# Optimization experiments

Measured on AMD Instinct MI355X. Metric: run time of the kernel, lower is better.

The kernel has to match this reference:

```python
import jax, jax.numpy as jnp
import numpy as np

N_NODES = 50000
N_EDGES = 800000
D_IN, D_HID, D_OUT = 128, 256, 128


def _glorot(key, shape):
    fan_in, fan_out = shape[1], shape[0]
    lim = (6.0 / (fan_in + fan_out)) ** 0.5
    return jax.random.uniform(key, shape, jnp.float32, -lim, lim)


def setup_inputs() -> dict:
    key = jax.random.key(0)
    ks = jax.random.split(key, 8)
    x = jax.random.normal(ks[0], (N_NODES, D_IN), dtype=jnp.float32)
    edge_index = jax.random.randint(ks[1], (2, N_EDGES), 0, N_NODES, dtype=jnp.int64)
    # Layer 1: SAGEConv(D_IN -> D_HID); Layer 2: SAGEConv(D_HID -> D_OUT)
    # PyG SAGEConv: out = lin_l(mean_aggr(x_j)) + lin_r(x); bias lives in lin_l.
    Wl1 = _glorot(ks[2], (D_HID, D_IN))
    bl1 = jnp.zeros((D_HID,), jnp.float32)
    Wr1 = _glorot(ks[3], (D_HID, D_IN))
    Wl2 = _glorot(ks[4], (D_OUT, D_HID))
    bl2 = jnp.zeros((D_OUT,), jnp.float32)
    Wr2 = _glorot(ks[5], (D_OUT, D_HID))
    return {"x": x, "Wl1": Wl1, "bl1": bl1, "Wr1": Wr1,
            "Wl2": Wl2, "bl2": bl2, "Wr2": Wr2, "edge_index": edge_index}


def _sage_conv(x, src, dst, deg_inv, Wl, bl, Wr):
    # gather source features per edge, sum into dst buckets, normalize by in-degree
    msg_sum = jax.ops.segment_sum(x[src], dst, num_segments=N_NODES)  # [N, d_in]
    mean = msg_sum * deg_inv  # mean aggregation; isolated nodes -> zeros
    return mean @ Wl.T + bl + x @ Wr.T


def reference(x, Wl1, bl1, Wr1, Wl2, bl2, Wr2, edge_index):
    src, dst = edge_index[0], edge_index[1]
    deg = jax.ops.segment_sum(jnp.ones((N_EDGES,), jnp.float32), dst,
                              num_segments=N_NODES)
    deg_inv = (1.0 / jnp.maximum(deg, 1.0))[:, None]  # [N, 1]
    h = _sage_conv(x, src, dst, deg_inv, Wl1, bl1, Wr1)
    h = jax.nn.relu(h)  # dropout is identity in eval mode
    out = _sage_conv(h, src, dst, deg_inv, Wl2, bl2, Wr2)
    return out
```

## Files before the change

kernel.cpp:

```cpp
#include <hip/hip_runtime.h>
#include <hip/hip_fp16.h>

#define N_NODES 50000
#define N_EDGES 800000
#define D_IN 128
#define D_HID 256
#define D_OUT 128
#define NCHUNK 196
#define GEMM_GRID 512

typedef _Float16 f16x8 __attribute__((ext_vector_type(8)));
typedef float f32x4 __attribute__((ext_vector_type(4)));


__device__ __forceinline__ void cvt8(const float* __restrict__ src,
                                     __half* __restrict__ dstp, int i) {
    const float4* s4 = (const float4*)src;
    float4 a = s4[i * 2];
    float4 b = s4[i * 2 + 1];
    float4 o;
    __half2* op = (__half2*)&o;
    op[0] = __float22half2_rn(make_float2(a.x, a.y));
    op[1] = __float22half2_rn(make_float2(a.z, a.w));
    op[2] = __float22half2_rn(make_float2(b.x, b.y));
    op[3] = __float22half2_rn(make_float2(b.z, b.w));
    ((float4*)dstp)[i] = o;
}

__global__ __launch_bounds__(256)
void prep_kernel(const float* __restrict__ x, __half* __restrict__ xb,
                 const float* __restrict__ Wl1, const float* __restrict__ Wr1,
                 const float* __restrict__ Wl2, const float* __restrict__ Wr2,
                 __half* __restrict__ wl1h, __half* __restrict__ wr1h,
                 __half* __restrict__ wl2h, __half* __restrict__ wr2h,
                 int* __restrict__ deg) {
    int b = blockIdx.x;
    if (b < 3125) {
        int i = b * 256 + threadIdx.x;
        cvt8(x, xb, i);
    } else if (b < 3141) {
        int i = (b - 3125) * 256 + threadIdx.x;
        cvt8(Wl1, wl1h, i);
        cvt8(Wr1, wr1h, i);
        cvt8(Wl2, wl2h, i);
        cvt8(Wr2, wr2h, i);
    } else {
        int i = (b - 3141) * 256 + threadIdx.x;
        if (i < N_NODES) deg[i] = 0;
    }
}


__global__ void deg_rank_kernel(const int* __restrict__ dst, int* __restrict__ deg,
                                int* __restrict__ rank) {
    int i = blockIdx.x * blockDim.x + threadIdx.x;
    if (i < N_EDGES) rank[i] = atomicAdd(&deg[dst[i]], 1);
}

__global__ void chunk_sum(const int* __restrict__ deg, int* __restrict__ partial) {
    __shared__ int s[256];
    int i = blockIdx.x * 256 + threadIdx.x;
    s[threadIdx.x] = (i < N_NODES) ? deg[i] : 0;
    __syncthreads();
    for (int off = 128; off > 0; off >>= 1) {
        if (threadIdx.x < off) s[threadIdx.x] += s[threadIdx.x + off];
        __syncthreads();
    }
    if (threadIdx.x == 0) partial[blockIdx.x] = s[0];
}

__global__ void scatter_scan(const int* __restrict__ deg, const int* __restrict__ partial,
                             int* __restrict__ row_ptr, float* __restrict__ deg_inv) {
    __shared__ int s[256];
    __shared__ int base_s;
    const int tid = threadIdx.x;
    const int bid = blockIdx.x;
    s[tid] = (tid < bid) ? partial[tid] : 0;
    __syncthreads();
    for (int off = 128; off > 0; off >>= 1) {
        if (tid < off) s[tid] += s[tid + off];
        __syncthreads();
    }
    if (tid == 0) base_s = s[0];
    __syncthreads();
    int i = bid * 256 + tid;
    int v = (i < N_NODES) ? deg[i] : 0;
    s[tid] = v;
    __syncthreads();
    for (int off = 1; off < 256; off <<= 1) {
        int t = (tid >= off) ? s[tid - off] : 0;
        __syncthreads();
        s[tid] += t;
        __syncthreads();
    }
    if (i < N_NODES) {
        int rp = base_s + s[tid] - v;
        row_ptr[i] = rp;
        deg_inv[i] = 1.0f / fmaxf((float)v, 1.0f);
        if (i == N_NODES - 1) row_ptr[N_NODES] = N_EDGES;
    }
}

__global__ void fill_csr(const int* __restrict__ src, const int* __restrict__ dst,
                         const int* __restrict__ rank, const int* __restrict__ row_ptr,
                         int* __restrict__ csr_src) {
    int e = blockIdx.x * blockDim.x + threadIdx.x;
    if (e < N_EDGES) {
        csr_src[row_ptr[dst[e]] + rank[e]] = src[e];
    }
}


__device__ __forceinline__ void add_row(const float4& v, float2 (&acc)[4]) {
    const __half2* hp = (const __half2*)&v;
    #pragma unroll
    for (int j = 0; j < 4; ++j) {
        float2 f = __half22float2(hp[j]);
        acc[j].x += f.x;
        acc[j].y += f.y;
    }
}

template<bool ACCUM_F32>
__device__ __forceinline__ void gather_core(const __half2* __restrict__ feat,
                                            const int* __restrict__ row_ptr,
                                            const int* __restrict__ csr_src,
                                            const float* __restrict__ deg_inv,
                                            __half2* __restrict__ outh,
                                            float* __restrict__ outf) {
    const float4* feat4 = (const float4*)feat;
    const int lane = threadIdx.x & 63;
    const int g = lane >> 4;
    const int s = lane & 15;
    const int n = blockIdx.x * 4 + (threadIdx.x >> 6);
    const int beg = row_ptr[n];
    const int end = row_ptr[n + 1];
    float2 acc[4] = {};

    int idx = (beg + lane < end) ? csr_src[beg + lane] : 0;
    int base = beg;
    while (base < end) {
        int cnt = end - base;
        if (cnt > 64) cnt = 64;
        const int nbase = base + 64;
        int nidx = (nbase + lane < end) ? csr_src[nbase + lane] : 0;

        int it = 0;
        for (; it + 16 <= cnt; it += 16) {
            int s0 = __shfl(idx, it + g);
            int s1 = __shfl(idx, it + 4 + g);
            int s2 = __shfl(idx, it + 8 + g);
            int s3 = __shfl(idx, it + 12 + g);
            float4 v0 = feat4[(size_t)s0 * 16 + s];
            float4 v1 = feat4[(size_t)s1 * 16 + s];
            float4 v2 = feat4[(size_t)s2 * 16 + s];
            float4 v3 = feat4[(size_t)s3 * 16 + s];
            add_row(v0, acc);
            add_row(v1, acc);
            add_row(v2, acc);
            add_row(v3, acc);
        }
        for (; it + 4 <= cnt; it += 4) {
            int s0 = __shfl(idx, it + g);
            float4 v0 = feat4[(size_t)s0 * 16 + s];
            add_row(v0, acc);
        }
        if (it < cnt) {
            int s0 = __shfl(idx, it + g);
            if (g < cnt - it) {
                float4 v0 = feat4[(size_t)s0 * 16 + s];
                add_row(v0, acc);
            }
        }
        idx = nidx;
        base = nbase;
    }

    #pragma unroll
    for (int j = 0; j < 4; ++j) {
        acc[j].x += __shfl_xor(acc[j].x, 16);
        acc[j].y += __shfl_xor(acc[j].y, 16);
        acc[j].x += __shfl_xor(acc[j].x, 32);
        acc[j].y += __shfl_xor(acc[j].y, 32);
    }
    if (g == 0) {
        float di = deg_inv[n];
        if (ACCUM_F32) {
            float4* orow = (float4*)(outf + (size_t)n * 128);
            float4 o0 = orow[s * 2];
            float4 o1 = orow[s * 2 + 1];
            o0.x += acc[0].x * di; o0.y += acc[0].y * di;
            o0.z += acc[1].x * di; o0.w += acc[1].y * di;
            o1.x += acc[2].x * di; o1.y += acc[2].y * di;
            o1.z += acc[3].x * di; o1.w += acc[3].y * di;
            orow[s * 2] = o0;
            orow[s * 2 + 1] = o1;
        } else {
            float4 o;
            __half2* op = (__half2*)&o;
            op[0] = __float22half2_rn(make_float2(acc[0].x * di, acc[0].y * di));
            op[1] = __float22half2_rn(make_float2(acc[1].x * di, acc[1].y * di));
            op[2] = __float22half2_rn(make_float2(acc[2].x * di, acc[2].y * di));
            op[3] = __float22half2_rn(make_float2(acc[3].x * di, acc[3].y * di));
            ((float4*)(outh + (size_t)n * 64))[s] = o;
        }
    }
}

__global__ __launch_bounds__(256)
void gather_mean_h(const __half2* __restrict__ feat, const int* __restrict__ row_ptr,
                   const int* __restrict__ csr_src, const float* __restrict__ deg_inv,
                   __half2* __restrict__ outv) {
    gather_core<false>(feat, row_ptr, csr_src, deg_inv, outv, nullptr);
}

__global__ __launch_bounds__(256)
void gather_mean_add_f32(const __half2* __restrict__ feat, const int* __restrict__ row_ptr,
                         const int* __restrict__ csr_src, const float* __restrict__ deg_inv,
                         float* __restrict__ out) {
    gather_core<true>(feat, row_ptr, csr_src, deg_inv, nullptr, out);
}


#define HPAD 264

__global__ __launch_bounds__(256, 1)
void gemm_fused(const __half* __restrict__ Aa, const __half* __restrict__ Ba,
                const __half* __restrict__ Ab, const __half* __restrict__ Bb,
                const float* __restrict__ bias1,
                const __half* __restrict__ B20, const __half* __restrict__ B21,
                const float* __restrict__ bias2,
                __half* __restrict__ P, float* __restrict__ out) {
    __shared__ __half hlds[2][16][HPAD];
    const int lane = threadIdx.x & 63;
    const int wave = threadIdx.x >> 6;
    const int quad = lane >> 4;
    const int l16 = lane & 15;
    const int koff = quad * 8;

    f16x8 bf1[2][4][4];
    #pragma unroll
    for (int p = 0; p < 2; ++p) {
        const __half* __restrict__ B = p ? Bb : Ba;
        #pragma unroll
        for (int kc = 0; kc < 4; ++kc)
            #pragma unroll
            for (int nt = 0; nt < 4; ++nt)
                bf1[p][kc][nt] = *(const f16x8*)(
                    B + (size_t)(wave * 64 + nt * 16 + l16) * D_IN + kc * 32 + koff);
    }
    float bv1[4];
    #pragma unroll
    for (int nt = 0; nt < 4; ++nt) bv1[nt] = bias1[wave * 64 + nt * 16 + l16];

    f16x8 bf20[8][2], bf21[8][2];
    #pragma unroll
    for (int kc = 0; kc < 8; ++kc)
        #pragma unroll
        for (int nt = 0; nt < 2; ++nt) {
            size_t brow = (size_t)(wave * 32 + nt * 16 + l16) * D_HID + kc * 32 + koff;
            bf20[kc][nt] = *(const f16x8*)(B20 + brow);
            bf21[kc][nt] = *(const f16x8*)(B21 + brow);
        }
    float bv2[2];
    #pragma unroll
    for (int nt = 0; nt < 2; ++nt) bv2[nt] = bias2[wave * 32 + nt * 16 + l16];

    const int NT = N_NODES / 16;
    const int g = gridDim.x;

    auto loadA = [&](int t, f16x8 (&a)[2][4]) {
        const size_t arow = (size_t)(t * 16 + l16) * D_IN + koff;
        #pragma unroll
        for (int kc = 0; kc < 4; ++kc) {
            a[0][kc] = *(const f16x8*)(Aa + arow + kc * 32);
            a[1][kc] = *(const f16x8*)(Ab + arow + kc * 32);
        }
    };

    auto step = [&](int tile, const f16x8 (&a)[2][4], int buf) {
        f32x4 acc1[4] = {};
        #pragma unroll
        for (int p = 0; p < 2; ++p)
            #pragma unroll
            for (int kc = 0; kc < 4; ++kc)
                #pragma unroll
                for (int nt = 0; nt < 4; ++nt)
                    acc1[nt] = __builtin_amdgcn_mfma_f32_16x16x32_f16(
                        a[p][kc], bf1[p][kc][nt], acc1[nt], 0, 0, 0);
        #pragma unroll
        for (int nt = 0; nt < 4; ++nt) {
            int col = wave * 64 + nt * 16 + l16;
            #pragma unroll
            for (int r = 0; r < 4; ++r)
                hlds[buf][quad * 4 + r][col] =
                    __float2half(fmaxf(acc1[nt][r] + bv1[nt], 0.f));
        }
        __syncthreads();
        f32x4 acc20[2] = {};
        f32x4 acc21[2] = {};
        #pragma unroll
        for (int kc = 0; kc < 8; ++kc) {
            f16x8 a2 = *(const f16x8*)&hlds[buf][l16][kc * 32 + koff];
            #pragma unroll
            for (int nt = 0; nt < 2; ++nt) {
                acc20[nt] = __builtin_amdgcn_mfma_f32_16x16x32_f16(
                    a2, bf20[kc][nt], acc20[nt], 0, 0, 0);
                acc21[nt] = __builtin_amdgcn_mfma_f32_16x16x32_f16(
                    a2, bf21[kc][nt], acc21[nt], 0, 0, 0);
            }
        }
        #pragma unroll
        for (int nt = 0; nt < 2; ++nt) {
            int col = wave * 32 + nt * 16 + l16;
            #pragma unroll
            for (int r = 0; r < 4; ++r) {
                int row = tile * 16 + quad * 4 + r;
                P[(size_t)row * D_OUT + col] = __float2half(acc20[nt][r]);
                out[(size_t)row * D_OUT + col] = acc21[nt][r] + bv2[nt];
            }
        }
    };

    f16x8 A0[2][4], A1[2][4];
    int tile = blockIdx.x;
    int buf = 0;
    loadA(tile, A0);
    while (true) {
        if (tile + g < NT) loadA(tile + g, A1);
        step(tile, A0, buf);
        buf ^= 1;
        tile += g;
        if (tile >= NT) break;
        if (tile + g < NT) loadA(tile + g, A0);
        step(tile, A1, buf);
        buf ^= 1;
        tile += g;
        if (tile >= NT) break;
    }
}

extern "C" void kernel_launch(void* const* d_in, const int* in_sizes, int n_in,
                              void* d_out, int out_size, void* d_ws, size_t ws_size,
                              hipStream_t stream) {
    const float* x   = (const float*)d_in[0];
    const float* Wl1 = (const float*)d_in[1];
    const float* bl1 = (const float*)d_in[2];
    const float* Wr1 = (const float*)d_in[3];
    const float* Wl2 = (const float*)d_in[4];
    const float* bl2 = (const float*)d_in[5];
    const float* Wr2 = (const float*)d_in[6];
    const int*   ei  = (const int*)d_in[7];
    const int* src = ei;
    const int* dst = ei + N_EDGES;
    float* out = (float*)d_out;

    char* w = (char*)d_ws;
    auto alloc = [&](size_t bytes) {
        char* r = w;
        w += (bytes + 255) & ~(size_t)255;
        return r;
    };
    int*     deg       = (int*)alloc((size_t)N_NODES * 4);
    int*     row_ptr   = (int*)alloc((size_t)(N_NODES + 1) * 4);
    int*     rank      = (int*)alloc((size_t)N_EDGES * 4);
    int*     partial   = (int*)alloc(NCHUNK * 4);
    int*     csr_src   = (int*)alloc((size_t)N_EDGES * 4);
    float*   deg_inv   = (float*)alloc((size_t)N_NODES * 4);
    __half2* xb        = (__half2*)alloc((size_t)N_NODES * 64 * 4);
    __half2* mean1     = (__half2*)alloc((size_t)N_NODES * 64 * 4);
    __half2* pb        = (__half2*)alloc((size_t)N_NODES * 64 * 4);
    __half*  wl1h      = (__half*)alloc(4 * 32768 * 2);
    __half*  wr1h = wl1h + 32768;
    __half*  wl2h = wr1h + 32768;
    __half*  wr2h = wl2h + 32768;

    prep_kernel<<<3337, 256, 0, stream>>>(x, (__half*)xb, Wl1, Wr1, Wl2, Wr2,
        wl1h, wr1h, wl2h, wr2h, deg);

    deg_rank_kernel<<<(N_EDGES + 255) / 256, 256, 0, stream>>>(dst, deg, rank);
    chunk_sum<<<NCHUNK, 256, 0, stream>>>(deg, partial);
    scatter_scan<<<NCHUNK, 256, 0, stream>>>(deg, partial, row_ptr, deg_inv);
    fill_csr<<<(N_EDGES + 255) / 256, 256, 0, stream>>>(src, dst, rank, row_ptr, csr_src);

    gather_mean_h<<<12500, 256, 0, stream>>>(xb, row_ptr, csr_src, deg_inv, mean1);

    gemm_fused<<<GEMM_GRID, 256, 0, stream>>>(
        (const __half*)mean1, wl1h, (const __half*)xb, wr1h, bl1,
        wl2h, wr2h, bl2, (__half*)pb, out);

    gather_mean_add_f32<<<12500, 256, 0, stream>>>(pb, row_ptr, csr_src, deg_inv, out);
}
```

Measured before the change: 239.4 us.

## Fuse layer-1 mean gather into the fused GEMM kernel via per-tile CSR gather

```diff
diff --git a/kernel.cpp b/kernel.cpp
--- a/kernel.cpp
+++ b/kernel.cpp
@@ -7,7 +7,8 @@
 #define D_HID 256
 #define D_OUT 128
 #define NCHUNK 196
-#define GEMM_GRID 512
+#define NTILES 3125
+#define FUSED_GRID 256
 
 typedef _Float16 f16x8 __attribute__((ext_vector_type(8)));
 typedef float f32x4 __attribute__((ext_vector_type(4)));
@@ -121,13 +122,11 @@
     }
 }
 
-template<bool ACCUM_F32>
-__device__ __forceinline__ void gather_core(const __half2* __restrict__ feat,
-                                            const int* __restrict__ row_ptr,
-                                            const int* __restrict__ csr_src,
-                                            const float* __restrict__ deg_inv,
-                                            __half2* __restrict__ outh,
-                                            float* __restrict__ outf) {
+
+__global__ __launch_bounds__(256)
+void gather_mean_add_f32(const __half2* __restrict__ feat, const int* __restrict__ row_ptr,
+                         const int* __restrict__ csr_src, const float* __restrict__ deg_inv,
+                         float* __restrict__ out) {
     const float4* feat4 = (const float4*)feat;
     const int lane = threadIdx.x & 63;
     const int g = lane >> 4;
@@ -185,158 +184,208 @@
     }
     if (g == 0) {
         float di = deg_inv[n];
-        if (ACCUM_F32) {
-            float4* orow = (float4*)(outf + (size_t)n * 128);
-            float4 o0 = orow[s * 2];
-            float4 o1 = orow[s * 2 + 1];
-            o0.x += acc[0].x * di; o0.y += acc[0].y * di;
-            o0.z += acc[1].x * di; o0.w += acc[1].y * di;
-            o1.x += acc[2].x * di; o1.y += acc[2].y * di;
-            o1.z += acc[3].x * di; o1.w += acc[3].y * di;
-            orow[s * 2] = o0;
-            orow[s * 2 + 1] = o1;
-        } else {
-            float4 o;
-            __half2* op = (__half2*)&o;
-            op[0] = __float22half2_rn(make_float2(acc[0].x * di, acc[0].y * di));
-            op[1] = __float22half2_rn(make_float2(acc[1].x * di, acc[1].y * di));
-            op[2] = __float22half2_rn(make_float2(acc[2].x * di, acc[2].y * di));
-            op[3] = __float22half2_rn(make_float2(acc[3].x * di, acc[3].y * di));
-            ((float4*)(outh + (size_t)n * 64))[s] = o;
-        }
-    }
-}
-
-__global__ __launch_bounds__(256)
-void gather_mean_h(const __half2* __restrict__ feat, const int* __restrict__ row_ptr,
-                   const int* __restrict__ csr_src, const float* __restrict__ deg_inv,
-                   __half2* __restrict__ outv) {
-    gather_core<false>(feat, row_ptr, csr_src, deg_inv, outv, nullptr);
-}
-
-__global__ __launch_bounds__(256)
-void gather_mean_add_f32(const __half2* __restrict__ feat, const int* __restrict__ row_ptr,
-                         const int* __restrict__ csr_src, const float* __restrict__ deg_inv,
-                         float* __restrict__ out) {
-    gather_core<true>(feat, row_ptr, csr_src, deg_inv, nullptr, out);
-}
-
-
-#define HPAD 264
-
-__global__ __launch_bounds__(256, 1)
-void gemm_fused(const __half* __restrict__ Aa, const __half* __restrict__ Ba,
-                const __half* __restrict__ Ab, const __half* __restrict__ Bb,
+        float4* orow = (float4*)(out + (size_t)n * 128);
+        float4 o0 = orow[s * 2];
+        float4 o1 = orow[s * 2 + 1];
+        o0.x += acc[0].x * di; o0.y += acc[0].y * di;
+        o0.z += acc[1].x * di; o0.w += acc[1].y * di;
+        o1.x += acc[2].x * di; o1.y += acc[2].y * di;
+        o1.z += acc[3].x * di; o1.w += acc[3].y * di;
+        orow[s * 2] = o0;
+        orow[s * 2 + 1] = o1;
+    }
+}
+
+
+__global__ __launch_bounds__(512, 2)
+void sage_fused(const __half* __restrict__ xb,
+                const __half* __restrict__ Wl1h, const __half* __restrict__ Wr1h,
                 const float* __restrict__ bias1,
                 const __half* __restrict__ B20, const __half* __restrict__ B21,
                 const float* __restrict__ bias2,
+                const int* __restrict__ row_ptr, const int* __restrict__ csr_src,
+                const float* __restrict__ deg_inv,
                 __half* __restrict__ P, float* __restrict__ out) {
-    __shared__ __half hlds[2][16][HPAD];
+    __shared__ __half ldsA[16][136];
+    __shared__ __half ldsH[16][264];
+    const float4* feat4 = (const float4*)xb;
     const int lane = threadIdx.x & 63;
     const int wave = threadIdx.x >> 6;
     const int quad = lane >> 4;
     const int l16 = lane & 15;
     const int koff = quad * 8;
 
-    f16x8 bf1[2][4][4];
+    f16x8 bf1[2][4][2];
     #pragma unroll
     for (int p = 0; p < 2; ++p) {
-        const __half* __restrict__ B = p ? Bb : Ba;
+        const __half* __restrict__ B = p ? Wr1h : Wl1h;
         #pragma unroll
         for (int kc = 0; kc < 4; ++kc)
             #pragma unroll
-            for (int nt = 0; nt < 4; ++nt)
+            for (int nt = 0; nt < 2; ++nt)
                 bf1[p][kc][nt] = *(const f16x8*)(
-                    B + (size_t)(wave * 64 + nt * 16 + l16) * D_IN + kc * 32 + koff);
-    }
-    float bv1[4];
+                    B + (size_t)(wave * 32 + nt * 16 + l16) * D_IN + kc * 32 + koff);
+    }
+    float bv1[2];
     #pragma unroll
-    for (int nt = 0; nt < 4; ++nt) bv1[nt] = bias1[wave * 64 + nt * 16 + l16];
-
-    f16x8 bf20[8][2], bf21[8][2];
+    for (int nt = 0; nt < 2; ++nt) bv1[nt] = bias1[wave * 32 + nt * 16 + l16];
+
+    f16x8 bf20[8], bf21[8];
     #pragma unroll
-    for (int kc = 0; kc < 8; ++kc)
-        #pragma unroll
-        for (int nt = 0; nt < 2; ++nt) {
-            size_t brow = (size_t)(wave * 32 + nt * 16 + l16) * D_HID + kc * 32 + koff;
-            bf20[kc][nt] = *(const f16x8*)(B20 + brow);
-            bf21[kc][nt] = *(const f16x8*)(B21 + brow);
-        }
-    float bv2[2];
-    #pragma unroll
-    for (int nt = 0; nt < 2; ++nt) bv2[nt] = bias2[wave * 32 + nt * 16 + l16];
-
-    const int NT = N_NODES / 16;
-    const int g = gridDim.x;
-
-    auto loadA = [&](int t, f16x8 (&a)[2][4]) {
-        const size_t arow = (size_t)(t * 16 + l16) * D_IN + koff;
+    for (int kc = 0; kc < 8; ++kc) {
+        size_t brow = (size_t)(wave * 16 + l16) * D_HID + kc * 32 + koff;
+        bf20[kc] = *(const f16x8*)(B20 + brow);
+        bf21[kc] = *(const f16x8*)(B21 + brow);
+    }
+    float bv2 = bias2[wave * 16 + l16];
+
+    for (int tile = blockIdx.x; tile < NTILES; tile += gridDim.x) {
+        f16x8 ax[4];
+        const size_t arow = (size_t)(tile * 16 + l16) * D_IN + koff;
+        #pragma unroll
+        for (int kc = 0; kc < 4; ++kc)
+            ax[kc] = *(const f16x8*)(xb + arow + kc * 32);
+
+        {
+            const int nb = tile * 16 + wave * 2;
+            int rp = row_ptr[nb + (lane < 2 ? lane : 2)];
+            float dv = (lane < 2) ? deg_inv[nb + lane] : 0.f;
+            const int spanBeg = __shfl(rp, 0);
+            const int spanEnd = __shfl(rp, 2);
+            int i0 = (spanBeg + lane < spanEnd) ? csr_src[spanBeg + lane] : 0;
+            int i1 = (spanBeg + 64 + lane < spanEnd) ? csr_src[spanBeg + 64 + lane] : 0;
+
+            #pragma unroll
+            for (int i = 0; i < 2; ++i) {
+                const int b = __shfl(rp, i);
+                const int e = __shfl(rp, i + 1);
+                float2 acc[4] = {};
+                if (e - spanBeg <= 128) {
+                    const int off = b - spanBeg;
+                    const int cnt = e - b;
+                    int it = 0;
+                    for (; it + 16 <= cnt; it += 16) {
+                        int p0 = off + it + quad;
+                        int p1 = p0 + 4, p2 = p0 + 8, p3 = p0 + 12;
+                        int a0 = __shfl(i0, p0 & 63), b0 = __shfl(i1, p0 & 63);
+                        int a1 = __shfl(i0, p1 & 63), b1 = __shfl(i1, p1 & 63);
+                        int a2 = __shfl(i0, p2 & 63), b2 = __shfl(i1, p2 & 63);
+                        int a3 = __shfl(i0, p3 & 63), b3 = __shfl(i1, p3 & 63);
+                        int s0 = p0 < 64 ? a0 : b0;
+                        int s1 = p1 < 64 ? a1 : b1;
+                        int s2 = p2 < 64 ? a2 : b2;
+                        int s3 = p3 < 64 ? a3 : b3;
+                        float4 v0 = feat4[(size_t)s0 * 16 + l16];
+                        float4 v1 = feat4[(size_t)s1 * 16 + l16];
+                        float4 v2 = feat4[(size_t)s2 * 16 + l16];
+                        float4 v3 = feat4[(size_t)s3 * 16 + l16];
+                        add_row(v0, acc);
+                        add_row(v1, acc);
+                        add_row(v2, acc);
+                        add_row(v3, acc);
+                    }
+                    for (; it + 4 <= cnt; it += 4) {
+                        int p0 = off + it + quad;
+                        int a0 = __shfl(i0, p0 & 63), b0 = __shfl(i1, p0 & 63);
+                        int s0 = p0 < 64 ? a0 : b0;
+                        float4 v0 = feat4[(size_t)s0 * 16 + l16];
+                        add_row(v0, acc);
+                    }
+                    if (it < cnt) {
+                        int p0 = off + it + quad;
+                        int a0 = __shfl(i0, p0 & 63), b0 = __shfl(i1, p0 & 63);
+                        int s0 = p0 < 64 ? a0 : b0;
+                        if (quad < cnt - it) {
+                            float4 v0 = feat4[(size_t)s0 * 16 + l16];
+                            add_row(v0, acc);
+                        }
+                    }
+                } else {
+                    int it = b;
+                    for (; it + 16 <= e; it += 16) {
+                        int s0 = csr_src[it + quad];
+                        int s1 = csr_src[it + 4 + quad];
+                        int s2 = csr_src[it + 8 + quad];
+                        int s3 = csr_src[it + 12 + quad];
+                        float4 v0 = feat4[(size_t)s0 * 16 + l16];
+                        float4 v1 = feat4[(size_t)s1 * 16 + l16];
+                        float4 v2 = feat4[(size_t)s2 * 16 + l16];
+                        float4 v3 = feat4[(size_t)s3 * 16 + l16];
+                        add_row(v0, acc);
+                        add_row(v1, acc);
+                        add_row(v2, acc);
+                        add_row(v3, acc);
+                    }
+                    for (; it + 4 <= e; it += 4) {
+                        int s0 = csr_src[it + quad];
+                        float4 v0 = feat4[(size_t)s0 * 16 + l16];
+                        add_row(v0, acc);
+                    }
+                    if (it < e) {
+                        if (quad < e - it) {
+                            int s0 = csr_src[it + quad];
+                            float4 v0 = feat4[(size_t)s0 * 16 + l16];
+                            add_row(v0, acc);
+                        }
+                    }
+                }
+                #pragma unroll
+                for (int j = 0; j < 4; ++j) {
+                    acc[j].x += __shfl_xor(acc[j].x, 16);
+                    acc[j].y += __shfl_xor(acc[j].y, 16);
+                    acc[j].x += __shfl_xor(acc[j].x, 32);
+                    acc[j].y += __shfl_xor(acc[j].y, 32);
+                }
+                if (quad == 0) {
+                    float di = __shfl(dv, i);
+                    float4 o;
+                    __half2* op = (__half2*)&o;
+                    op[0] = __float22half2_rn(make_float2(acc[0].x * di, acc[0].y * di));
+                    op[1] = __float22half2_rn(make_float2(acc[1].x * di, acc[1].y * di));
+                    op[2] = __float22half2_rn(make_float2(acc[2].x * di, acc[2].y * di));
+                    op[3] = __float22half2_rn(make_float2(acc[3].x * di, acc[3].y * di));
+                    *(float4*)&ldsA[wave * 2 + i][l16 * 8] = o;
+                }
+            }
+        }
+        __syncthreads();
+
+        f32x4 acc1[2] = {};
         #pragma unroll
         for (int kc = 0; kc < 4; ++kc) {
-            a[0][kc] = *(const f16x8*)(Aa + arow + kc * 32);
-            a[1][kc] = *(const f16x8*)(Ab + arow + kc * 32);
-        }
-    };
-
-    auto step = [&](int tile, const f16x8 (&a)[2][4], int buf) {
-        f32x4 acc1[4] = {};
-        #pragma unroll
-        for (int p = 0; p < 2; ++p)
-            #pragma unroll
-            for (int kc = 0; kc < 4; ++kc)
-                #pragma unroll
-                for (int nt = 0; nt < 4; ++nt)
-                    acc1[nt] = __builtin_amdgcn_mfma_f32_16x16x32_f16(
-                        a[p][kc], bf1[p][kc][nt], acc1[nt], 0, 0, 0);
-        #pragma unroll
-        for (int nt = 0; nt < 4; ++nt) {
-            int col = wave * 64 + nt * 16 + l16;
-            #pragma unroll
-            for (int r = 0; r < 4; ++r)
-                hlds[buf][quad * 4 + r][col] =
-                    __float2half(fmaxf(acc1[nt][r] + bv1[nt], 0.f));
-        }
-        __syncthreads();
-        f32x4 acc20[2] = {};
-        f32x4 acc21[2] = {};
-        #pragma unroll
-        for (int kc = 0; kc < 8; ++kc) {
-            f16x8 a2 = *(const f16x8*)&hlds[buf][l16][kc * 32 + koff];
+            f16x8 am = *(const f16x8*)&ldsA[l16][kc * 32 + koff];
             #pragma unroll
             for (int nt = 0; nt < 2; ++nt) {
-                acc20[nt] = __builtin_amdgcn_mfma_f32_16x16x32_f16(
-                    a2, bf20[kc][nt], acc20[nt], 0, 0, 0);
-                acc21[nt] = __builtin_amdgcn_mfma_f32_16x16x32_f16(
-                    a2, bf21[kc][nt], acc21[nt], 0, 0, 0);
+                acc1[nt] = __builtin_amdgcn_mfma_f32_16x16x32_f16(
+                    am, bf1[0][kc][nt], acc1[nt], 0, 0, 0);
+                acc1[nt] = __builtin_amdgcn_mfma_f32_16x16x32_f16(
+                    ax[kc], bf1[1][kc][nt], acc1[nt], 0, 0, 0);
             }
         }
         #pragma unroll
         for (int nt = 0; nt < 2; ++nt) {
             int col = wave * 32 + nt * 16 + l16;
             #pragma unroll
-            for (int r = 0; r < 4; ++r) {
-                int row = tile * 16 + quad * 4 + r;
-                P[(size_t)row * D_OUT + col] = __float2half(acc20[nt][r]);
-                out[(size_t)row * D_OUT + col] = acc21[nt][r] + bv2[nt];
-            }
-        }
-    };
-
-    f16x8 A0[2][4], A1[2][4];
-    int tile = blockIdx.x;
-    int buf = 0;
-    loadA(tile, A0);
-    while (true) {
-        if (tile + g < NT) loadA(tile + g, A1);
-        step(tile, A0, buf);
-        buf ^= 1;
-        tile += g;
-        if (tile >= NT) break;
-        if (tile + g < NT) loadA(tile + g, A0);
-        step(tile, A1, buf);
-        buf ^= 1;
-        tile += g;
-        if (tile >= NT) break;
+            for (int r = 0; r < 4; ++r)
+                ldsH[quad * 4 + r][col] =
+                    __float2half(fmaxf(acc1[nt][r] + bv1[nt], 0.f));
+        }
+        __syncthreads();
+
+        f32x4 acc20 = {}, acc21 = {};
+        #pragma unroll
+        for (int kc = 0; kc < 8; ++kc) {
+            f16x8 a2 = *(const f16x8*)&ldsH[l16][kc * 32 + koff];
+            acc20 = __builtin_amdgcn_mfma_f32_16x16x32_f16(a2, bf20[kc], acc20, 0, 0, 0);
+            acc21 = __builtin_amdgcn_mfma_f32_16x16x32_f16(a2, bf21[kc], acc21, 0, 0, 0);
+        }
+        const int col = wave * 16 + l16;
+        #pragma unroll
+        for (int r = 0; r < 4; ++r) {
+            int row = tile * 16 + quad * 4 + r;
+            P[(size_t)row * D_OUT + col] = __float2half(acc20[r]);
+            out[(size_t)row * D_OUT + col] = acc21[r] + bv2;
+        }
     }
 }
 
@@ -368,7 +417,6 @@
     int*     csr_src   = (int*)alloc((size_t)N_EDGES * 4);
     float*   deg_inv   = (float*)alloc((size_t)N_NODES * 4);
     __half2* xb        = (__half2*)alloc((size_t)N_NODES * 64 * 4);
-    __half2* mean1     = (__half2*)alloc((size_t)N_NODES * 64 * 4);
     __half2* pb        = (__half2*)alloc((size_t)N_NODES * 64 * 4);
     __half*  wl1h      = (__half*)alloc(4 * 32768 * 2);
     __half*  wr1h = wl1h + 32768;
@@ -383,11 +431,9 @@
     scatter_scan<<<NCHUNK, 256, 0, stream>>>(deg, partial, row_ptr, deg_inv);
     fill_csr<<<(N_EDGES + 255) / 256, 256, 0, stream>>>(src, dst, rank, row_ptr, csr_src);
 
-    gather_mean_h<<<12500, 256, 0, stream>>>(xb, row_ptr, csr_src, deg_inv, mean1);
-
-    gemm_fused<<<GEMM_GRID, 256, 0, stream>>>(
-        (const __half*)mean1, wl1h, (const __half*)xb, wr1h, bl1,
-        wl2h, wr2h, bl2, (__half*)pb, out);
+    sage_fused<<<FUSED_GRID, 512, 0, stream>>>(
+        (const __half*)xb, wl1h, wr1h, bl1, wl2h, wr2h, bl2,
+        row_ptr, csr_src, deg_inv, (__half*)pb, out);
 
     gather_mean_add_f32<<<12500, 256, 0, stream>>>(pb, row_ptr, csr_src, deg_inv, out);
 }
```

Result: slower. 260.7 us (+8.9%).

## Split fused GEMM across 8 waves with smaller per-wave weight tiles

Applied to the files above, without the earlier changes.

```diff
diff --git a/kernel.cpp b/kernel.cpp
--- a/kernel.cpp
+++ b/kernel.cpp
@@ -7,6 +7,7 @@
 #define D_HID 256
 #define D_OUT 128
 #define NCHUNK 196
+#define NTILES 3125
 #define GEMM_GRID 512
 
 typedef _Float16 f16x8 __attribute__((ext_vector_type(8)));
@@ -224,119 +225,106 @@
 
 #define HPAD 264
 
-__global__ __launch_bounds__(256, 1)
-void gemm_fused(const __half* __restrict__ Aa, const __half* __restrict__ Ba,
-                const __half* __restrict__ Ab, const __half* __restrict__ Bb,
-                const float* __restrict__ bias1,
-                const __half* __restrict__ B20, const __half* __restrict__ B21,
-                const float* __restrict__ bias2,
-                __half* __restrict__ P, float* __restrict__ out) {
-    __shared__ __half hlds[2][16][HPAD];
+__global__ __launch_bounds__(512, 2)
+void gemm_fused2(const __half* __restrict__ Aa,
+                 const __half* __restrict__ Ab,
+                 const __half* __restrict__ Wl1h, const __half* __restrict__ Wr1h,
+                 const float* __restrict__ bias1,
+                 const __half* __restrict__ B20, const __half* __restrict__ B21,
+                 const float* __restrict__ bias2,
+                 __half* __restrict__ P, float* __restrict__ out) {
+    __shared__ __half ldsH[16][HPAD];
     const int lane = threadIdx.x & 63;
     const int wave = threadIdx.x >> 6;
     const int quad = lane >> 4;
     const int l16 = lane & 15;
     const int koff = quad * 8;
 
-    f16x8 bf1[2][4][4];
+    f16x8 bf1[2][4][2];
     #pragma unroll
     for (int p = 0; p < 2; ++p) {
-        const __half* __restrict__ B = p ? Bb : Ba;
+        const __half* __restrict__ B = p ? Wr1h : Wl1h;
         #pragma unroll
         for (int kc = 0; kc < 4; ++kc)
             #pragma unroll
-            for (int nt = 0; nt < 4; ++nt)
+            for (int nt = 0; nt < 2; ++nt)
                 bf1[p][kc][nt] = *(const f16x8*)(
-                    B + (size_t)(wave * 64 + nt * 16 + l16) * D_IN + kc * 32 + koff);
-    }
-    float bv1[4];
-    #pragma unroll
-    for (int nt = 0; nt < 4; ++nt) bv1[nt] = bias1[wave * 64 + nt * 16 + l16];
-
-    f16x8 bf20[8][2], bf21[8][2];
-    #pragma unroll
-    for (int kc = 0; kc < 8; ++kc)
-        #pragma unroll
-        for (int nt = 0; nt < 2; ++nt) {
-            size_t brow = (size_t)(wave * 32 + nt * 16 + l16) * D_HID + kc * 32 + koff;
-            bf20[kc][nt] = *(const f16x8*)(B20 + brow);
-            bf21[kc][nt] = *(const f16x8*)(B21 + brow);
-        }
-    float bv2[2];
-    #pragma unroll
-    for (int nt = 0; nt < 2; ++nt) bv2[nt] = bias2[wave * 32 + nt * 16 + l16];
-
-    const int NT = N_NODES / 16;
+                    B + (size_t)(wave * 32 + nt * 16 + l16) * D_IN + kc * 32 + koff);
+    }
+    float bv1[2];
+    #pragma unroll
+    for (int nt = 0; nt < 2; ++nt) bv1[nt] = bias1[wave * 32 + nt * 16 + l16];
+
+    f16x8 bf20[8], bf21[8];
+    #pragma unroll
+    for (int kc = 0; kc < 8; ++kc) {
+        size_t brow = (size_t)(wave * 16 + l16) * D_HID + kc * 32 + koff;
+        bf20[kc] = *(const f16x8*)(B20 + brow);
+        bf21[kc] = *(const f16x8*)(B21 + brow);
+    }
+    float bv2 = bias2[wave * 16 + l16];
+
     const int g = gridDim.x;
 
-    auto loadA = [&](int t, f16x8 (&a)[2][4]) {
+    auto loadA = [&](int t, f16x8 (&am)[4], f16x8 (&ax)[4]) {
         const size_t arow = (size_t)(t * 16 + l16) * D_IN + koff;
         #pragma unroll
         for (int kc = 0; kc < 4; ++kc) {
-            a[0][kc] = *(const f16x8*)(Aa + arow + kc * 32);
-            a[1][kc] = *(const f16x8*)(Ab + arow + kc * 32);
+            am[kc] = *(const f16x8*)(Aa + arow + kc * 32);
+            ax[kc] = *(const f16x8*)(Ab + arow + kc * 32);
         }
     };
 
-    auto step = [&](int tile, const f16x8 (&a)[2][4], int buf) {
-        f32x4 acc1[4] = {};
-        #pragma unroll
-        for (int p = 0; p < 2; ++p)
-            #pragma unroll
-            for (int kc = 0; kc < 4; ++kc)
-                #pragma unroll
-                for (int nt = 0; nt < 4; ++nt)
-                    acc1[nt] = __builtin_amdgcn_mfma_f32_16x16x32_f16(
-                        a[p][kc], bf1[p][kc][nt], acc1[nt], 0, 0, 0);
-        #pragma unroll
-        for (int nt = 0; nt < 4; ++nt) {
-            int col = wave * 64 + nt * 16 + l16;
-            #pragma unroll
-            for (int r = 0; r < 4; ++r)
-                hlds[buf][quad * 4 + r][col] =
-                    __float2half(fmaxf(acc1[nt][r] + bv1[nt], 0.f));
-        }
-        __syncthreads();
-        f32x4 acc20[2] = {};
-        f32x4 acc21[2] = {};
-        #pragma unroll
-        for (int kc = 0; kc < 8; ++kc) {
-            f16x8 a2 = *(const f16x8*)&hlds[buf][l16][kc * 32 + koff];
+    auto step = [&](int tile, const f16x8 (&am)[4], const f16x8 (&ax)[4]) {
+        f32x4 acc1[2] = {};
+        #pragma unroll
+        for (int kc = 0; kc < 4; ++kc)
             #pragma unroll
             for (int nt = 0; nt < 2; ++nt) {
-                acc20[nt] = __builtin_amdgcn_mfma_f32_16x16x32_f16(
-                    a2, bf20[kc][nt], acc20[nt], 0, 0, 0);
-                acc21[nt] = __builtin_amdgcn_mfma_f32_16x16x32_f16(
-                    a2, bf21[kc][nt], acc21[nt], 0, 0, 0);
+                acc1[nt] = __builtin_amdgcn_mfma_f32_16x16x32_f16(
+                    am[kc], bf1[0][kc][nt], acc1[nt], 0, 0, 0);
+                acc1[nt] = __builtin_amdgcn_mfma_f32_16x16x32_f16(
+                    ax[kc], bf1[1][kc][nt], acc1[nt], 0, 0, 0);
             }
-        }
+        __syncthreads();
         #pragma unroll
         for (int nt = 0; nt < 2; ++nt) {
             int col = wave * 32 + nt * 16 + l16;
             #pragma unroll
-            for (int r = 0; r < 4; ++r) {
-                int row = tile * 16 + quad * 4 + r;
-                P[(size_t)row * D_OUT + col] = __float2half(acc20[nt][r]);
-                out[(size_t)row * D_OUT + col] = acc21[nt][r] + bv2[nt];
-            }
+            for (int r = 0; r < 4; ++r)
+                ldsH[quad * 4 + r][col] =
+                    __float2half(fmaxf(acc1[nt][r] + bv1[nt], 0.f));
+        }
+        __syncthreads();
+        f32x4 acc20 = {}, acc21 = {};
+        #pragma unroll
+        for (int kc = 0; kc < 8; ++kc) {
+            f16x8 a2 = *(const f16x8*)&ldsH[l16][kc * 32 + koff];
+            acc20 = __builtin_amdgcn_mfma_f32_16x16x32_f16(a2, bf20[kc], acc20, 0, 0, 0);
+            acc21 = __builtin_amdgcn_mfma_f32_16x16x32_f16(a2, bf21[kc], acc21, 0, 0, 0);
+        }
+        const int col = wave * 16 + l16;
+        #pragma unroll
+        for (int r = 0; r < 4; ++r) {
+            int row = tile * 16 + quad * 4 + r;
+            P[(size_t)row * D_OUT + col] = __float2half(acc20[r]);
+            out[(size_t)row * D_OUT + col] = acc21[r] + bv2;
         }
     };
 
-    f16x8 A0[2][4], A1[2][4];
+    f16x8 am0[4], ax0[4], am1[4], ax1[4];
     int tile = blockIdx.x;
-    int buf = 0;
-    loadA(tile, A0);
+    if (tile >= NTILES) return;
+    loadA(tile, am0, ax0);
     while (true) {
-        if (tile + g < NT) loadA(tile + g, A1);
-        step(tile, A0, buf);
-        buf ^= 1;
+        if (tile + g < NTILES) loadA(tile + g, am1, ax1);
+        step(tile, am0, ax0);
         tile += g;
-        if (tile >= NT) break;
-        if (tile + g < NT) loadA(tile + g, A0);
-        step(tile, A1, buf);
-        buf ^= 1;
+        if (tile >= NTILES) break;
+        if (tile + g < NTILES) loadA(tile + g, am0, ax0);
+        step(tile, am1, ax1);
         tile += g;
-        if (tile >= NT) break;
+        if (tile >= NTILES) break;
     }
 }
 
@@ -385,8 +373,8 @@
 
     gather_mean_h<<<12500, 256, 0, stream>>>(xb, row_ptr, csr_src, deg_inv, mean1);
 
-    gemm_fused<<<GEMM_GRID, 256, 0, stream>>>(
-        (const __half*)mean1, wl1h, (const __half*)xb, wr1h, bl1,
+    gemm_fused2<<<GEMM_GRID, 512, 0, stream>>>(
+        (const __half*)mean1, (const __half*)xb, wl1h, wr1h, bl1,
         wl2h, wr2h, bl2, (__half*)pb, out);
 
     gather_mean_add_f32<<<12500, 256, 0, stream>>>(pb, row_ptr, csr_src, deg_inv, out);
```

Result: slower. 248.9 us (+3.9%).

## Merge chunk_sum into scatter_scan and software-pipeline fused GEMM stages

Applied to the files above, without the earlier changes.

```diff
diff --git a/kernel.cpp b/kernel.cpp
--- a/kernel.cpp
+++ b/kernel.cpp
@@ -7,6 +7,7 @@
 #define D_HID 256
 #define D_OUT 128
 #define NCHUNK 196
+#define NTILES 3125
 #define GEMM_GRID 512
 
 typedef _Float16 f16x8 __attribute__((ext_vector_type(8)));
@@ -57,25 +58,16 @@
     if (i < N_EDGES) rank[i] = atomicAdd(&deg[dst[i]], 1);
 }
 
-__global__ void chunk_sum(const int* __restrict__ deg, int* __restrict__ partial) {
-    __shared__ int s[256];
-    int i = blockIdx.x * 256 + threadIdx.x;
-    s[threadIdx.x] = (i < N_NODES) ? deg[i] : 0;
-    __syncthreads();
-    for (int off = 128; off > 0; off >>= 1) {
-        if (threadIdx.x < off) s[threadIdx.x] += s[threadIdx.x + off];
-        __syncthreads();
-    }
-    if (threadIdx.x == 0) partial[blockIdx.x] = s[0];
-}
-
-__global__ void scatter_scan(const int* __restrict__ deg, const int* __restrict__ partial,
+
+__global__ void scatter_scan(const int* __restrict__ deg,
                              int* __restrict__ row_ptr, float* __restrict__ deg_inv) {
     __shared__ int s[256];
     __shared__ int base_s;
     const int tid = threadIdx.x;
     const int bid = blockIdx.x;
-    s[tid] = (tid < bid) ? partial[tid] : 0;
+    int sum = 0;
+    for (int j = tid; j < bid * 256; j += 256) sum += deg[j];
+    s[tid] = sum;
     __syncthreads();
     for (int off = 128; off > 0; off >>= 1) {
         if (tid < off) s[tid] += s[tid + off];
@@ -225,12 +217,12 @@
 #define HPAD 264
 
 __global__ __launch_bounds__(256, 1)
-void gemm_fused(const __half* __restrict__ Aa, const __half* __restrict__ Ba,
-                const __half* __restrict__ Ab, const __half* __restrict__ Bb,
-                const float* __restrict__ bias1,
-                const __half* __restrict__ B20, const __half* __restrict__ B21,
-                const float* __restrict__ bias2,
-                __half* __restrict__ P, float* __restrict__ out) {
+void gemm_fused3(const __half* __restrict__ Aa, const __half* __restrict__ Ba,
+                 const __half* __restrict__ Ab, const __half* __restrict__ Bb,
+                 const float* __restrict__ bias1,
+                 const __half* __restrict__ B20, const __half* __restrict__ B21,
+                 const float* __restrict__ bias2,
+                 __half* __restrict__ P, float* __restrict__ out) {
     __shared__ __half hlds[2][16][HPAD];
     const int lane = threadIdx.x & 63;
     const int wave = threadIdx.x >> 6;
@@ -266,7 +258,6 @@
     #pragma unroll
     for (int nt = 0; nt < 2; ++nt) bv2[nt] = bias2[wave * 32 + nt * 16 + l16];
 
-    const int NT = N_NODES / 16;
     const int g = gridDim.x;
 
     auto loadA = [&](int t, f16x8 (&a)[2][4]) {
@@ -278,7 +269,7 @@
         }
     };
 
-    auto step = [&](int tile, const f16x8 (&a)[2][4], int buf) {
+    auto produce = [&](const f16x8 (&a)[2][4], int buf) {
         f32x4 acc1[4] = {};
         #pragma unroll
         for (int p = 0; p < 2; ++p)
@@ -296,7 +287,9 @@
                 hlds[buf][quad * 4 + r][col] =
                     __float2half(fmaxf(acc1[nt][r] + bv1[nt], 0.f));
         }
-        __syncthreads();
+    };
+
+    auto consume = [&](int tile, int buf) {
         f32x4 acc20[2] = {};
         f32x4 acc21[2] = {};
         #pragma unroll
@@ -323,20 +316,25 @@
     };
 
     f16x8 A0[2][4], A1[2][4];
-    int tile = blockIdx.x;
+    int t = blockIdx.x;
     int buf = 0;
-    loadA(tile, A0);
+    loadA(t, A0);
+    produce(A0, 0);
+    if (t + g < NTILES) loadA(t + g, A1);
     while (true) {
-        if (tile + g < NT) loadA(tile + g, A1);
-        step(tile, A0, buf);
-        buf ^= 1;
-        tile += g;
-        if (tile >= NT) break;
-        if (tile + g < NT) loadA(tile + g, A0);
-        step(tile, A1, buf);
-        buf ^= 1;
-        tile += g;
-        if (tile >= NT) break;
+        __syncthreads();
+        consume(t, buf);
+        if (t + g >= NTILES) break;
+        produce(A1, buf ^ 1);
+        if (t + 2 * g < NTILES) loadA(t + 2 * g, A0);
+        t += g; buf ^= 1;
+
+        __syncthreads();
+        consume(t, buf);
+        if (t + g >= NTILES) break;
+        produce(A0, buf ^ 1);
+        if (t + 2 * g < NTILES) loadA(t + 2 * g, A1);
+        t += g; buf ^= 1;
     }
 }
 
@@ -364,7 +362,6 @@
     int*     deg       = (int*)alloc((size_t)N_NODES * 4);
     int*     row_ptr   = (int*)alloc((size_t)(N_NODES + 1) * 4);
     int*     rank      = (int*)alloc((size_t)N_EDGES * 4);
-    int*     partial   = (int*)alloc(NCHUNK * 4);
     int*     csr_src   = (int*)alloc((size_t)N_EDGES * 4);
     float*   deg_inv   = (float*)alloc((size_t)N_NODES * 4);
     __half2* xb        = (__half2*)alloc((size_t)N_NODES * 64 * 4);
@@ -379,13 +376,12 @@
         wl1h, wr1h, wl2h, wr2h, deg);
 
     deg_rank_kernel<<<(N_EDGES + 255) / 256, 256, 0, stream>>>(dst, deg, rank);
-    chunk_sum<<<NCHUNK, 256, 0, stream>>>(deg, partial);
-    scatter_scan<<<NCHUNK, 256, 0, stream>>>(deg, partial, row_ptr, deg_inv);
+    scatter_scan<<<NCHUNK, 256, 0, stream>>>(deg, row_ptr, deg_inv);
     fill_csr<<<(N_EDGES + 255) / 256, 256, 0, stream>>>(src, dst, rank, row_ptr, csr_src);
 
     gather_mean_h<<<12500, 256, 0, stream>>>(xb, row_ptr, csr_src, deg_inv, mean1);
 
-    gemm_fused<<<GEMM_GRID, 256, 0, stream>>>(
+    gemm_fused3<<<GEMM_GRID, 256, 0, stream>>>(
         (const __half*)mean1, wl1h, (const __half*)xb, wr1h, bl1,
         wl2h, wr2h, bl2, (__half*)pb, out);
 
```

Measured after the change: 262.1 us. 9.5% more time.
